# Optimization experiments

Measured on AMD Instinct MI355X. Metric: run time of the kernel, lower is better.

The kernel has to match this reference:

```python
import jax, jax.numpy as jnp
import numpy as np

B, L, C_IN = 32, 8192, 64
K, F = 3, 128


def setup_inputs() -> dict:
    key = jax.random.key(0)
    k1, k2 = jax.random.split(key)
    x = jax.random.normal(k1, (B, L, C_IN), dtype=jnp.float32)
    # glorot-ish scale for the conv kernel [k, C_in, F] (TF WIO layout)
    w = jax.random.normal(k2, (K, C_IN, F), dtype=jnp.float32) * (2.0 / (K * C_IN + F)) ** 0.5
    b = jnp.zeros((F,), dtype=jnp.float32)
    return {"x": x, "w": w, "b": b}


def reference(x, w, b):
    # Original: per-position matmul+trace == valid conv1d; then bias + relu.
    # x: [B, L, C_in], w: [K, C_in, F] -> out: [B, L-K+1, F]
    out = jax.lax.conv_general_dilated(
        x, w,
        window_strides=(1,),
        padding="VALID",
        dimension_numbers=("NWC", "WIO", "NWC"),
    )
    return jax.nn.relu(out + b)
```

## Files before the change

### kernel.cpp

```cpp
#include <hip/hip_runtime.h>
#include <hip/hip_bf16.h>

typedef __attribute__((ext_vector_type(8))) short short8;
typedef __attribute__((ext_vector_type(4))) float floatx4;

#define B_SZ   32
#define L_IN   8192
#define C_INCH 64
#define KW     3
#define F_OUT  128
#define L_OUT  (L_IN - KW + 1)
#define KDIM   (KW * C_INCH)

#define TILE_L  64
#define AROWS   (TILE_L + 2)
#define NGRID   (B_SZ * (L_IN / TILE_L))

#define XCHUNKS (AROWS * 16)

#define WTAB_ELEMS (8 * 6 * 64)

__device__ __forceinline__ unsigned pk2(float a, float b) {
    __hip_bfloat162 h = __float22bfloat162_rn(make_float2(a, b));
    unsigned u;
    __builtin_memcpy(&u, &h, 4);
    return u;
}

__global__ __launch_bounds__(256) void w_prep(const float* __restrict__ w,
                                              short8* __restrict__ wtab) {
    int id = blockIdx.x * 256 + threadIdx.x;
    if (id >= WTAB_ELEMS) return;
    int lane = id & 63;
    int s    = (id >> 6) % 6;
    int nt   = id / 384;
    int nl = lane & 15, q = lane >> 4;
    const float* __restrict__ wf = w + nt * 16 + nl;
    float t[8];
#pragma unroll
    for (int j = 0; j < 8; ++j) t[j] = wf[(s * 32 + q * 8 + j) * F_OUT];
    union { unsigned u[4]; short8 v; } hb;
    hb.u[0] = pk2(t[0], t[1]);
    hb.u[1] = pk2(t[2], t[3]);
    hb.u[2] = pk2(t[4], t[5]);
    hb.u[3] = pk2(t[6], t[7]);
    wtab[id] = hb.v;
}

template <bool PREP>
__global__ __launch_bounds__(256, 4) void conv1d_mfma(const float* __restrict__ x,
                                                      const float* __restrict__ w,
                                                      const float* __restrict__ bias,
                                                      float* __restrict__ out,
                                                      const short8* __restrict__ wtab) {
    __shared__ __align__(16) float a_raw[AROWS * C_INCH];

    const int tid  = threadIdx.x;
    const int lane = tid & 63;
    const int wave = tid >> 6;
    const int q    = lane >> 4;
    const int nl   = lane & 15;

    const int g  = blockIdx.x;
    const int b  = g >> 7;
    const int l0 = (g & 127) * TILE_L;

    short8 bfrag[6][2];
    if (PREP) {
#pragma unroll
        for (int n = 0; n < 2; ++n)
#pragma unroll
            for (int s = 0; s < 6; ++s)
                bfrag[s][n] = wtab[(((wave * 2 + n) * 6 + s) << 6) + lane];
    } else {
#pragma unroll
        for (int n = 0; n < 2; ++n) {
            const int f = (wave * 2 + n) * 16 + nl;
            const float* __restrict__ wf = w + f;
#pragma unroll
            for (int s = 0; s < 6; ++s) {
                float t[8];
#pragma unroll
                for (int j = 0; j < 8; ++j)
                    t[j] = wf[(s * 32 + q * 8 + j) * F_OUT];
                union { unsigned u[4]; short8 v; } hb;
                hb.u[0] = pk2(t[0], t[1]);
                hb.u[1] = pk2(t[2], t[3]);
                hb.u[2] = pk2(t[4], t[5]);
                hb.u[3] = pk2(t[6], t[7]);
                bfrag[s][n] = hb.v;
            }
        }
    }

    float4 bv[2];
#pragma unroll
    for (int n = 0; n < 2; ++n)
        bv[n] = *(const float4*)(bias + (wave * 2 + n) * 16 + q * 4);

#pragma unroll
    for (int r = 0; r < 5; ++r) {
        int c = r * 256 + tid;
        if (c < XCHUNKS) {
            int row = c >> 4;
            int pc  = c & 15;
            int spc = pc ^ (row & 7);
            int grow = b * L_IN + l0 + row;
            grow = grow < (B_SZ * L_IN - 1) ?
                   grow : (B_SZ * L_IN - 1);
            const float* src = x + (size_t)grow * C_INCH + spc * 4;
            float* dst = &a_raw[(r * 256 + wave * 64) * 4];
            __builtin_amdgcn_global_load_lds(
                (const __attribute__((address_space(1))) void*)src,
                (__attribute__((address_space(3))) void*)dst, 16, 0, 0);
        }
    }
    __syncthreads();

    floatx4 acc[4][2];
#pragma unroll
    for (int m = 0; m < 4; ++m)
#pragma unroll
        for (int n = 0; n < 2; ++n) acc[m][n] = (floatx4){0.f, 0.f, 0.f, 0.f};

#pragma unroll
    for (int s = 0; s < 6; ++s) {
#pragma unroll
        for (int m = 0; m < 4; ++m) {
            const int row = m * 16 + nl + (s >> 1);
            const int fxr = row & 7;
            const int pc0 = (s & 1) * 8 + q * 2;
            floatx4 c0 = *(const floatx4*)&a_raw[row * C_INCH + (pc0 ^ fxr) * 4];
            floatx4 c1 = *(const floatx4*)&a_raw[row * C_INCH + ((pc0 + 1) ^ fxr) * 4];
            union { unsigned u[4]; short8 v; } h;
            h.u[0] = pk2(c0[0], c0[1]);
            h.u[1] = pk2(c0[2], c0[3]);
            h.u[2] = pk2(c1[0], c1[1]);
            h.u[3] = pk2(c1[2], c1[3]);
#pragma unroll
            for (int n = 0; n < 2; ++n)
                acc[m][n] = __builtin_amdgcn_mfma_f32_16x16x32_bf16(
                    bfrag[s][n], h.v, acc[m][n], 0, 0, 0);
        }
    }

#pragma unroll
    for (int n = 0; n < 2; ++n) {
        const int fb = (wave * 2 + n) * 16 + q * 4;
#pragma unroll
        for (int m = 0; m < 4; ++m) {
            const int l = l0 + m * 16 + nl;
            if (l < L_OUT) {
                float4 v;
                v.x = acc[m][n][0] + bv[n].x;
                v.y = acc[m][n][1] + bv[n].y;
                v.z = acc[m][n][2] + bv[n].z;
                v.w = acc[m][n][3] + bv[n].w;
                v.x = v.x > 0.f ? v.x : 0.f;
                v.y = v.y > 0.f ? v.y : 0.f;
                v.z = v.z > 0.f ? v.z : 0.f;
                v.w = v.w > 0.f ? v.w : 0.f;
                *(float4*)(out + ((size_t)b * L_OUT + l) * F_OUT + fb) = v;
            }
        }
    }
}

extern "C" void kernel_launch(void* const* d_in, const int* in_sizes, int n_in,
                              void* d_out, int out_size, void* d_ws, size_t ws_size,
                              hipStream_t stream) {
    const float* x    = (const float*)d_in[0];
    const float* w    = (const float*)d_in[1];
    const float* bias = (const float*)d_in[2];
    float* out        = (float*)d_out;

    if (d_ws != nullptr && ws_size >= (size_t)WTAB_ELEMS * sizeof(short8)) {
        short8* wtab = (short8*)d_ws;
        w_prep<<<dim3((WTAB_ELEMS + 255) / 256), 256, 0, stream>>>(w, wtab);
        conv1d_mfma<true><<<dim3(NGRID), 256, 0, stream>>>(x, w, bias, out, wtab);
    } else {
        conv1d_mfma<false><<<dim3(NGRID), 256, 0, stream>>>(x, w, bias, out, nullptr);
    }
}
```

Before: 193.1 us.

## Process two L-tiles per block with double-buffered LDS staging

Each block now computes two consecutive 64-row tiles, which halves the grid. Both tiles' input windows are issued up front into two LDS buffers. Partial vmcnt waits let the second tile's loads overlap the first tile's MFMA work and stores, and the per-block weight-fragment loads are amortized over twice the output. The cost is double the LDS per block, and correctness depends on hand-counted vmcnt values that also count the interleaved stores.

```diff
diff --git a/kernel.cpp b/kernel.cpp
--- a/kernel.cpp
+++ b/kernel.cpp
@@ -14,9 +14,8 @@
 
 #define TILE_L  64
 #define AROWS   (TILE_L + 2)
-#define NGRID   (B_SZ * (L_IN / TILE_L))
-
-#define XCHUNKS (AROWS * 16)
+#define TPB     2
+#define NGRID   (B_SZ * (L_IN / TILE_L) / TPB)
 
 #define WTAB_ELEMS (8 * 6 * 64)
 
@@ -53,7 +52,7 @@
                                                       const float* __restrict__ bias,
                                                       float* __restrict__ out,
                                                       const short8* __restrict__ wtab) {
-    __shared__ __align__(16) float a_raw[AROWS * C_INCH];
+    __shared__ __align__(16) float a_raw[2][AROWS * C_INCH];
 
     const int tid  = threadIdx.x;
     const int lane = tid & 63;
@@ -61,9 +60,9 @@
     const int q    = lane >> 4;
     const int nl   = lane & 15;
 
-    const int g  = blockIdx.x;
-    const int b  = g >> 7;
-    const int l0 = (g & 127) * TILE_L;
+    const int g      = blockIdx.x;
+    const int b      = g >> 6;
+    const int l_base = (g & 63) * (TPB * TILE_L);
 
     short8 bfrag[6][2];
     if (PREP) {
@@ -98,70 +97,97 @@
     for (int n = 0; n < 2; ++n)
         bv[n] = *(const float4*)(bias + (wave * 2 + n) * 16 + q * 4);
 
-#pragma unroll
-    for (int r = 0; r < 5; ++r) {
-        int c = r * 256 + tid;
-        if (c < XCHUNKS) {
+    auto stage = [&](float* dbuf, int l0) {
+#pragma unroll
+        for (int r = 0; r < 4; ++r) {
+            int c   = r * 256 + tid;
             int row = c >> 4;
             int pc  = c & 15;
             int spc = pc ^ (row & 7);
+            const float* src =
+                x + ((size_t)(b * L_IN + l0 + row)) * C_INCH + spc * 4;
+            float* dst = &dbuf[(r * 256 + wave * 64) * 4];
+            __builtin_amdgcn_global_load_lds(
+                (const __attribute__((address_space(1))) void*)src,
+                (__attribute__((address_space(3))) void*)dst, 16, 0, 0);
+        }
+        {
+            int row  = 64 + (lane >> 4);
+            int pc   = lane & 15;
+            int spc  = pc ^ (row & 7);
             int grow = b * L_IN + l0 + row;
             grow = grow < (B_SZ * L_IN - 1) ?
                    grow : (B_SZ * L_IN - 1);
             const float* src = x + (size_t)grow * C_INCH + spc * 4;
-            float* dst = &a_raw[(r * 256 + wave * 64) * 4];
-            __builtin_amdgcn_global_load_lds(
-                (const __attribute__((address_space(1))) void*)src,
-                (__attribute__((address_space(3))) void*)dst, 16, 0, 0);
-        }
-    }
-    __syncthreads();
-
-    floatx4 acc[4][2];
-#pragma unroll
-    for (int m = 0; m < 4; ++m)
-#pragma unroll
-        for (int n = 0; n < 2; ++n) acc[m][n] = (floatx4){0.f, 0.f, 0.f, 0.f};
-
-#pragma unroll
-    for (int s = 0; s < 6; ++s) {
-#pragma unroll
-        for (int m = 0; m < 4; ++m) {
-            const int row = m * 16 + nl + (s >> 1);
-            const int fxr = row & 7;
-            const int pc0 = (s & 1) * 8 + q * 2;
-            floatx4 c0 = *(const floatx4*)&a_raw[row * C_INCH + (pc0 ^ fxr) * 4];
-            floatx4 c1 = *(const floatx4*)&a_raw[row * C_INCH + ((pc0 + 1) ^ fxr) * 4];
-            union { unsigned u[4]; short8 v; } h;
-            h.u[0] = pk2(c0[0], c0[1]);
-            h.u[1] = pk2(c0[2], c0[3]);
-            h.u[2] = pk2(c1[0], c1[1]);
-            h.u[3] = pk2(c1[2], c1[3]);
-#pragma unroll
-            for (int n = 0; n < 2; ++n)
-                acc[m][n] = __builtin_amdgcn_mfma_f32_16x16x32_bf16(
-                    bfrag[s][n], h.v, acc[m][n], 0, 0, 0);
-        }
-    }
-
-#pragma unroll
-    for (int n = 0; n < 2; ++n) {
-        const int fb = (wave * 2 + n) * 16 + q * 4;
-#pragma unroll
-        for (int m = 0; m < 4; ++m) {
-            const int l = l0 + m * 16 + nl;
-            if (l < L_OUT) {
-                float4 v;
-                v.x = acc[m][n][0] + bv[n].x;
-                v.y = acc[m][n][1] + bv[n].y;
-                v.z = acc[m][n][2] + bv[n].z;
-                v.w = acc[m][n][3] + bv[n].w;
-                v.x = v.x > 0.f ? v.x : 0.f;
-                v.y = v.y > 0.f ? v.y : 0.f;
-                v.z = v.z > 0.f ? v.z : 0.f;
-                v.w = v.w > 0.f ? v.w : 0.f;
-                *(float4*)(out + ((size_t)b * L_OUT + l) * F_OUT + fb) = v;
+            float* dst = &dbuf[1024 * 4];
+            if (lane < 32)
+                __builtin_amdgcn_global_load_lds(
+                    (const __attribute__((address_space(1))) void*)src,
+                    (__attribute__((address_space(3))) void*)dst, 16, 0, 0);
+        }
+    };
+
+    stage(a_raw[0], l_base);
+    stage(a_raw[1], l_base + TILE_L);
+    asm volatile("s_waitcnt vmcnt(5)" ::: "memory");
+    __builtin_amdgcn_s_barrier();
+
+#pragma unroll
+    for (int t = 0; t < TPB; ++t) {
+        const float* buf = a_raw[t];
+        const int l0 = l_base + t * TILE_L;
+
+        floatx4 acc[4][2];
+#pragma unroll
+        for (int m = 0; m < 4; ++m)
+#pragma unroll
+            for (int n = 0; n < 2; ++n) acc[m][n] = (floatx4){0.f, 0.f, 0.f, 0.f};
+
+#pragma unroll
+        for (int s = 0; s < 6; ++s) {
+#pragma unroll
+            for (int m = 0; m < 4; ++m) {
+                const int row = m * 16 + nl + (s >> 1);
+                const int fxr = row & 7;
+                const int pc0 = (s & 1) * 8 + q * 2;
+                floatx4 c0 = *(const floatx4*)&buf[row * C_INCH + (pc0 ^ fxr) * 4];
+                floatx4 c1 = *(const floatx4*)&buf[row * C_INCH + ((pc0 + 1) ^ fxr) * 4];
+                union { unsigned u[4]; short8 v; } h;
+                h.u[0] = pk2(c0[0], c0[1]);
+                h.u[1] = pk2(c0[2], c0[3]);
+                h.u[2] = pk2(c1[0], c1[1]);
+                h.u[3] = pk2(c1[2], c1[3]);
+#pragma unroll
+                for (int n = 0; n < 2; ++n)
+                    acc[m][n] = __builtin_amdgcn_mfma_f32_16x16x32_bf16(
+                        bfrag[s][n], h.v, acc[m][n], 0, 0, 0);
             }
+        }
+
+#pragma unroll
+        for (int n = 0; n < 2; ++n) {
+            const int fb = (wave * 2 + n) * 16 + q * 4;
+#pragma unroll
+            for (int m = 0; m < 4; ++m) {
+                const int l = l0 + m * 16 + nl;
+                if (l < L_OUT) {
+                    float4 v;
+                    v.x = acc[m][n][0] + bv[n].x;
+                    v.y = acc[m][n][1] + bv[n].y;
+                    v.z = acc[m][n][2] + bv[n].z;
+                    v.w = acc[m][n][3] + bv[n].w;
+                    v.x = v.x > 0.f ? v.x : 0.f;
+                    v.y = v.y > 0.f ? v.y : 0.f;
+                    v.z = v.z > 0.f ? v.z : 0.f;
+                    v.w = v.w > 0.f ? v.w : 0.f;
+                    *(float4*)(out + ((size_t)b * L_OUT + l) * F_OUT + fb) = v;
+                }
+            }
+        }
+
+        if (t + 1 < TPB) {
+            asm volatile("s_waitcnt vmcnt(8)" ::: "memory");
+            __builtin_amdgcn_s_barrier();
         }
     }
 }
```

Result: no change. 192.8 us (-0.2%).
